# Optimization experiments

Measured on AMD Instinct MI355X. Metric: run time of the kernel, lower is better.

The kernel has to match this reference:

```python
import jax, jax.numpy as jnp
import numpy as np

NUM_C, BS, L, D, M = 4096, 32, 512, 128, 50
TA, TB, TC = 0.075, 0.088, 1.0  # triangular membership params


def setup_inputs() -> dict:
    key = jax.random.key(0)
    ks = jax.random.split(key, 16)
    g = lambda i, shape, s: jax.random.normal(ks[i], shape, jnp.float32) * s
    return {
        "q": jax.random.randint(ks[0], (BS, L), 0, NUM_C),
        "r": jax.random.randint(ks[1], (BS, L), 0, 2),
        "k_emb": g(2, (NUM_C, D), 1.0),
        "Mk": g(3, (M, D), (2.0 / D) ** 0.5),
        "Mv0": g(4, (M, D), (2.0 / D) ** 0.5),
        "f_W": g(5, (D, 2 * D), (1.0 / (2 * D)) ** 0.5),
        "f_b": jnp.zeros((D,), jnp.float32),
        "a_W": g(6, (D, NUM_C + D), (1.0 / (NUM_C + D)) ** 0.5),
        "a_b": jnp.zeros((D,), jnp.float32),
        "e_W": g(7, (D, D), (2.0 / D) ** 0.5),
        "e_b": jnp.zeros((D,), jnp.float32),
        "add_W": g(8, (D, D), (2.0 / D) ** 0.5),
        "add_b": jnp.zeros((D,), jnp.float32),
        "Wih": g(9, (4 * D, D), (1.0 / D) ** 0.5),
        "Whh": g(10, (4 * D, D), (1.0 / D) ** 0.5),
        "bih": jnp.zeros((4 * D,), jnp.float32),
        "bhh": jnp.zeros((4 * D,), jnp.float32),
        "p_W": g(11, (1, D), (1.0 / D) ** 0.5),
        "p_b": jnp.zeros((1,), jnp.float32),
    }


def _forward(q, r, k_emb, Mk, Mv0, f_W, f_b, a_W, a_b, e_W, e_b,
             add_W, add_b, Wih, Whh, bih, bhh, p_W, p_b):
    B, T = q.shape
    k = k_emb[q]                                    # (B,L,D) key embeddings
    # a_embed = Linear(num_c + dim_s, dim_s) on concat(one_hot(q)*r, f):
    # split the weight so the one-hot matmul becomes a gather.
    a_Wq, a_Wf = a_W[:, :NUM_C], a_W[:, NUM_C:]
    yq = a_Wq.T[q] * r[..., None].astype(k.dtype)   # (B,L,D)

    def mem_step(Mv, xs):
        k_t, yq_t = xs                              # (B,D), (B,D)
        w = jax.nn.softmax(k_t @ Mk.T, axis=1)      # (B,M) addressing
        read = jnp.einsum('bm,bmd->bd', w, Mv)      # weighted read
        f = jnp.tanh(jnp.concatenate([read, k_t], 1) @ f_W.T + f_b)
        y = yq_t + f @ a_Wf.T + a_b                 # write content
        e = jax.nn.sigmoid(y @ e_W.T + e_b)         # erase gate
        a = jnp.tanh(y @ add_W.T + add_b)           # add vector
        Mv = Mv * (1.0 - w[:, :, None] * e[:, None, :]) + w[:, :, None] * a[:, None, :]
        return Mv, (w, f)

    Mv0b = jnp.broadcast_to(Mv0, (B, M, D))
    _, (w_all, f_all) = jax.lax.scan(
        mem_step, Mv0b, (k.transpose(1, 0, 2), yq.transpose(1, 0, 2)))
    w_all = w_all.transpose(1, 0, 2)                # (B,L,M)
    f_all = f_all.transpose(1, 0, 2)                # (B,L,D)

    # triangular membership -> ternary identity vectors {0,1,2}
    tw = jnp.maximum(jnp.minimum((w_all - TA) / (TB - TA),
                                 (TC - w_all) / (TC - TB)), 0.0)
    iv = jnp.where(tw >= 0.6, 2.0, jnp.where(tw >= 0.1, 1.0, 0.0))
    sq = jnp.sum(iv * iv, axis=2)                   # (B,L)
    dist = sq[:, :, None] + sq[:, None, :] - 2.0 * jnp.einsum('bim,bjm->bij', iv, iv)
    NEG = jnp.float32(-1e32)
    dist = jnp.where(dist > 0.0, NEG, dist)
    ut = jnp.triu(jnp.ones((T, T), bool), k=0)      # mask j >= i
    dist = jnp.where(ut[None], NEG, dist)
    idx = jnp.arange(T * T, dtype=dist.dtype).reshape(T, T)
    final = dist + idx[None]                        # (B,L,L)
    matched = jnp.max(final, axis=2) >= 0.0         # (B,L) has identical prev step
    prev = jnp.argmax(final, axis=2)                # (B,L) most recent identical t'

    # hop-LSTM: reuse hidden/cell state of previous identical timestep
    barange = jnp.arange(B)
    h0 = jnp.zeros((B, D), k.dtype)
    H0 = jnp.zeros((T, B, D), k.dtype)

    def lstm_step(carry, xs):
        h, c, H, C = carry
        t, f_t, m_t, p_t = xs
        h_in = jnp.where(m_t[:, None], H[p_t, barange], h)
        c_in = jnp.where(m_t[:, None], C[p_t, barange], c)
        gates = f_t @ Wih.T + bih + h_in @ Whh.T + bhh
        i_g, f_g, g_g, o_g = jnp.split(gates, 4, axis=1)  # torch order i,f,g,o
        c_new = jax.nn.sigmoid(f_g) * c_in + jax.nn.sigmoid(i_g) * jnp.tanh(g_g)
        h_new = jax.nn.sigmoid(o_g) * jnp.tanh(c_new)
        return (h_new, c_new, H.at[t].set(h_new), C.at[t].set(c_new)), h_new

    _, h_all = jax.lax.scan(
        lstm_step, (h0, h0, H0, H0),
        (jnp.arange(T), f_all.transpose(1, 0, 2), matched.T, prev.T))
    h_all = h_all.transpose(1, 0, 2)                # (B,L,D)
    # dropout is identity in eval mode
    p = jax.nn.sigmoid(h_all @ p_W.T + p_b)[..., 0]  # (B,L)
    return p


def reference(q, r, k_emb, Mk, Mv0, f_W, f_b, a_W, a_b, e_W, e_b,
              add_W, add_b, Wih, Whh, bih, bhh, p_W, p_b):
    return _forward(q, r, k_emb, Mk, Mv0, f_W, f_b, a_W, a_b, e_W, e_b,
                    add_W, add_b, Wih, Whh, bih, bhh, p_W, p_b)
```

## Files before the change

### kernel.cpp

```cpp
#include <hip/hip_runtime.h>
#include <cstdint>
#include <cstddef>

#define NUM_C 4096
#define BB 32
#define TT 512
#define DD 128
#define MM 50

using ull = unsigned long long;

__device__ __forceinline__ float sigmoidf_(float x){ return 1.0f/(1.0f + expf(-x)); }

__device__ __forceinline__ float fexp2_(float x){ return __builtin_amdgcn_exp2f(x); }
__device__ __forceinline__ float frcp_(float x){ return __builtin_amdgcn_rcpf(x); }
__device__ __forceinline__ float fast_sig_(float x){
  return frcp_(1.0f + fexp2_(-1.44269504088896341f*x));
}
__device__ __forceinline__ float fast_tanh_(float x){
  float t = fexp2_(2.88539008177792681f*x);
  return 1.0f - 2.0f*frcp_(t + 1.0f);
}

__device__ __forceinline__ float quadSum_(float v){
  int t = __builtin_amdgcn_update_dpp(0, __float_as_int(v), 0xB1, 0xF, 0xF, true);
  v += __int_as_float(t);
  t = __builtin_amdgcn_update_dpp(0, __float_as_int(v), 0x4E, 0xF, 0xF, true);
  v += __int_as_float(t);
  return v;
}

__device__ __forceinline__ void barL_(){
  asm volatile("s_waitcnt lgkmcnt(0)\n\ts_barrier" ::: "memory");
}
__device__ __forceinline__ void waitVM_(){
  asm volatile("s_waitcnt vmcnt(0)" ::: "memory");
}

__global__ __launch_bounds__(256) void kPre(
    const int* __restrict__ q, const int* __restrict__ r,
    const float* __restrict__ k_emb, const float* __restrict__ Mk,
    const float* __restrict__ f_W, const float* __restrict__ f_b,
    const float* __restrict__ a_W, const float* __restrict__ a_b,
    float* __restrict__ wAll, ull* __restrict__ keyLo, ull* __restrict__ keyHi,
    float* __restrict__ fpre, float* __restrict__ ypre)
{
  const int b = blockIdx.y, t0 = blockIdx.x * 32, tid = threadIdx.x;
  __shared__ __align__(16) float sK[32*129];
  __shared__ int sQ[32];
  __shared__ int sR[32];
  __shared__ union UU {
    struct { float sMk[MM*129]; double sZ[32*MM]; } p2;
    float sW2[128*65];
  } u;

  if (tid < 32){ sQ[tid] = q[b*TT + t0 + tid]; sR[tid] = r[b*TT + t0 + tid]; }
  __syncthreads();
  for (int i = tid; i < 32*128; i += 256){
    int tl = i >> 7, j = i & 127;
    sK[tl*129 + j] = k_emb[(size_t)sQ[tl]*DD + j];
  }
  for (int i = tid; i < MM*128; i += 256){
    int m = i >> 7, j = i & 127;
    u.p2.sMk[m*129 + j] = Mk[i];
  }
  __syncthreads();

  for (int idx = tid; idx < 32*MM; idx += 256){
    int tl = idx / MM, m = idx - tl*MM;
    double z = 0.0;
    for (int j = 0; j < DD; j++)
      z += (double)sK[tl*129 + j] * (double)u.p2.sMk[m*129 + j];
    u.p2.sZ[tl*MM + m] = z;
  }
  __syncthreads();

  {
    int tl = tid >> 3, l8 = tid & 7;
    double zmax = -1e300;
    for (int m = l8; m < MM; m += 8) zmax = fmax(zmax, u.p2.sZ[tl*MM + m]);
    for (int s = 1; s < 8; s <<= 1) zmax = fmax(zmax, __shfl_xor(zmax, s));
    double se = 0.0;
    for (int m = l8; m < MM; m += 8){
      double e = exp(u.p2.sZ[tl*MM + m] - zmax);
      u.p2.sZ[tl*MM + m] = e;
      se += e;
    }
    for (int s = 1; s < 8; s <<= 1) se += __shfl_xor(se, s);
    double inv = 1.0 / se;
    ull klo = 0, khi = 0;
    for (int m = l8; m < MM; m += 8){
      double w = u.p2.sZ[tl*MM + m] * inv;
      wAll[((size_t)(b*TT + t0 + tl))*MM + m] = (float)w;
      double tw = fmin((w - 0.075)/(0.088 - 0.075), (1.0 - w)/(1.0 - 0.088));
      tw = fmax(tw, 0.0);
      ull iv = (tw >= 0.6) ? 2ull : ((tw >= 0.1) ? 1ull : 0ull);
      if (m < 32) klo |= iv << (2*m); else khi |= iv << (2*(m-32));
    }
    for (int s = 1; s < 8; s <<= 1){ klo |= __shfl_xor(klo, s); khi |= __shfl_xor(khi, s); }
    if (l8 == 0){ keyLo[b*TT + t0 + tl] = klo; keyHi[b*TT + t0 + tl] = khi; }
  }

  {
    const int dq = tid & 31, tq = tid >> 5;
    float acc[4][4];
    #pragma unroll
    for (int a = 0; a < 4; a++){ acc[a][0]=0.f; acc[a][1]=0.f; acc[a][2]=0.f; acc[a][3]=0.f; }
    for (int jh = 0; jh < 2; jh++){
      __syncthreads();
      for (int i = tid; i < 128*64; i += 256){
        int dd = i >> 6, jj = i & 63;
        u.sW2[dd*65 + jj] = f_W[dd*256 + 128 + jh*64 + jj];
      }
      __syncthreads();
      for (int jj = 0; jj < 64; jj++){
        float kv[4], wv[4];
        #pragma unroll
        for (int a = 0; a < 4; a++) kv[a] = sK[(tq*4 + a)*129 + jh*64 + jj];
        #pragma unroll
        for (int c = 0; c < 4; c++) wv[c] = u.sW2[(dq*4 + c)*65 + jj];
        #pragma unroll
        for (int a = 0; a < 4; a++){
          acc[a][0] += kv[a]*wv[0]; acc[a][1] += kv[a]*wv[1];
          acc[a][2] += kv[a]*wv[2]; acc[a][3] += kv[a]*wv[3];
        }
      }
    }
    #pragma unroll
    for (int a = 0; a < 4; a++){
      int tl = tq*4 + a;
      #pragma unroll
      for (int c = 0; c < 4; c++){
        int d = dq*4 + c;
        fpre[((size_t)(b*TT + t0 + tl))*DD + d] = acc[a][c] + f_b[d];
      }
    }
  }

  for (int i = tid; i < 32*DD; i += 256){
    int tl = i >> 7, d = i & 127;
    ypre[((size_t)(b*TT + t0 + tl))*DD + d] =
        a_W[(size_t)d*(NUM_C + DD) + sQ[tl]] * (float)sR[tl] + a_b[d];
  }
}

__global__ __launch_bounds__(256) void kInit(
    const float* __restrict__ e_W, const float* __restrict__ add_W,
    const float* __restrict__ a_W,
    float* __restrict__ Ge, float* __restrict__ Ga,
    const float* __restrict__ Wih, float* __restrict__ Wih4)
{
  const int bx = blockIdx.x, tid = threadIdx.x;
  if (bx < 128){
    __shared__ float se[128];
    __shared__ float sa[128];
    const int d = bx;
    if (tid < 128){
      se[tid] = e_W[(size_t)d*DD + tid];
      sa[tid] = add_W[(size_t)d*DD + tid];
    }
    __syncthreads();
    if (tid < 128){
      const int k = tid;
      float ge = 0.f, ga = 0.f;
      for (int j = 0; j < DD; j++){
        float af = a_W[(size_t)j*(NUM_C + DD) + NUM_C + k];
        ge += se[j]*af;
        ga += sa[j]*af;
      }
      Ge[(size_t)d*DD + k] = ge;
      Ga[(size_t)d*DD + k] = ga;
    }
  } else {
    int idx = (bx - 128)*256 + tid;
    int j = idx >> 7, k = idx & 127;
    Wih4[(size_t)(k >> 2)*2048 + j*4 + (k & 3)] = Wih[idx];
  }
}

__global__ __launch_bounds__(256) void kEA(
    const float* __restrict__ ypre, const float* __restrict__ e_W,
    const float* __restrict__ add_W, const float* __restrict__ e_b,
    const float* __restrict__ add_b, float* __restrict__ eapre)
{
  const int jt = blockIdx.x;
  const int rt = blockIdx.y;
  const int tid = threadIdx.x;
  __shared__ float sW[64*129];
  __shared__ float sF[32*129];
  for (int i = tid; i < 64*128; i += 256){
    int jj = i >> 7, k = i & 127;
    int j = jt*64 + jj;
    sW[jj*129 + k] = (j < 128) ? e_W[(size_t)j*DD + k] : add_W[(size_t)(j-128)*DD + k];
  }
  for (int i = tid; i < 32*128; i += 256){
    int rr = i >> 7, k = i & 127;
    sF[rr*129 + k] = ypre[(size_t)(rt*32 + rr)*DD + k];
  }
  __syncthreads();
  const int jq = tid & 31, rq = tid >> 5;
  float acc[4][2];
  #pragma unroll
  for (int a = 0; a < 4; a++){ acc[a][0] = 0.f; acc[a][1] = 0.f; }
  for (int k = 0; k < 128; k++){
    float fv[4], wv[2];
    #pragma unroll
    for (int a = 0; a < 4; a++) fv[a] = sF[(rq*4 + a)*129 + k];
    wv[0] = sW[(jq*2 + 0)*129 + k];
    wv[1] = sW[(jq*2 + 1)*129 + k];
    #pragma unroll
    for (int a = 0; a < 4; a++){ acc[a][0] += fv[a]*wv[0]; acc[a][1] += fv[a]*wv[1]; }
  }
  #pragma unroll
  for (int a = 0; a < 4; a++){
    int rowi = rt*32 + rq*4 + a;
    #pragma unroll
    for (int c = 0; c < 2; c++){
      int j = jt*64 + jq*2 + c;
      float bj = (j < 128) ? e_b[j] : add_b[j - 128];
      eapre[(size_t)rowi*256 + j] = acc[a][c] + bj;
    }
  }
}

__global__ __launch_bounds__(512, 2) __attribute__((amdgpu_waves_per_eu(2, 2)))
void kFused(
    const float* __restrict__ wAll, const float* __restrict__ fpre,
    const float* __restrict__ eapre, const float* __restrict__ f_W,
    const float* __restrict__ Ge, const float* __restrict__ Ga,
    const float* __restrict__ Mv0, float* __restrict__ fAll,
    const float* __restrict__ Wih4, const float* __restrict__ bih,
    const float* __restrict__ bhh, const ull* __restrict__ keyLo,
    const ull* __restrict__ keyHi, int* __restrict__ prevA,
    const float* __restrict__ Whh, float* __restrict__ Hh,
    float* __restrict__ Ch, float* __restrict__ gpre,
    const float* __restrict__ p_W, const float* __restrict__ p_b,
    float* __restrict__ out, int* __restrict__ prog)
{
  const int tid = threadIdx.x;
  const int b = blockIdx.x & 31;
  const size_t base = (size_t)b*TT;

  __shared__ __align__(16) union SU {
    struct {
      float bufR[144]; float bufF[144]; float sW9[9*52];
      float sF8[8*128]; float sEA8[8*256]; float fO8[8*128];
    } m;
    struct { float sFc[8*128]; ull slo[TT]; ull shi[TT]; } g;
    struct {
      float xh[2][144]; float gbuf[8*512]; int spv[TT];
      float hRing[8*128]; float cRing[8*128]; float pw[DD];
    } l;
  } su;

  if (blockIdx.x < 32){
    const int dd = tid >> 2, kc = tid & 3, m0 = kc*13;
    const int wslot = (dd >> 5)*36 + (dd & 31);

    float mv[13];
    #pragma unroll
    for (int i = 0; i < 13; i++){
      int m = m0 + i;
      mv[i] = (m < MM) ? Mv0[(size_t)m*DD + dd] : 0.f;
    }
    float wf[32], ge[32], ga[32];
    {
      const float4* p;
      p = reinterpret_cast<const float4*>(&f_W[dd*256 + kc*32]);
      #pragma unroll
      for (int i = 0; i < 8; i++){ float4 v = p[i]; wf[4*i]=v.x; wf[4*i+1]=v.y; wf[4*i+2]=v.z; wf[4*i+3]=v.w; }
      p = reinterpret_cast<const float4*>(&Ge[(size_t)dd*DD + kc*32]);
      #pragma unroll
      for (int i = 0; i < 8; i++){ float4 v = p[i]; ge[4*i]=v.x; ge[4*i+1]=v.y; ge[4*i+2]=v.z; ge[4*i+3]=v.w; }
      p = reinterpret_cast<const float4*>(&Ga[(size_t)dd*DD + kc*32]);
      #pragma unroll
      for (int i = 0; i < 8; i++){ float4 v = p[i]; ga[4*i]=v.x; ga[4*i+1]=v.y; ga[4*i+2]=v.z; ga[4*i+3]=v.w; }
    }

    const int rr0 = tid / 50, mm0 = tid - rr0*50;
    if (tid < 18){ int rr = tid >> 1; su.m.sW9[rr*52 + 50 + (tid & 1)] = 0.f; }

    float4 pF = {0.f,0.f,0.f,0.f}, pEA = {0.f,0.f,0.f,0.f};
    float pW = 0.f;
    if (tid < 256) pF = reinterpret_cast<const float4*>(&fpre[base*DD])[tid];
    pEA = reinterpret_cast<const float4*>(&eapre[base*256])[tid];
    if (tid < 450) pW = wAll[(base + rr0)*MM + mm0];

    float wreg[13];

    for (int ch = 0; ch < TT/8; ch++){
      const int t0 = ch*8;
      if (ch){
        if (tid < 256){
          float4 v = reinterpret_cast<const float4*>(su.m.fO8)[tid];
          float* dst = &fAll[(base + t0 - 8)*DD + tid*4];
          __hip_atomic_store(dst+0, v.x, __ATOMIC_RELAXED, __HIP_MEMORY_SCOPE_AGENT);
          __hip_atomic_store(dst+1, v.y, __ATOMIC_RELAXED, __HIP_MEMORY_SCOPE_AGENT);
          __hip_atomic_store(dst+2, v.z, __ATOMIC_RELAXED, __HIP_MEMORY_SCOPE_AGENT);
          __hip_atomic_store(dst+3, v.w, __ATOMIC_RELAXED, __HIP_MEMORY_SCOPE_AGENT);
        }
      }
      if (tid < 256) reinterpret_cast<float4*>(su.m.sF8)[tid] = pF;
      reinterpret_cast<float4*>(su.m.sEA8)[tid] = pEA;
      if (tid < 450) su.m.sW9[rr0*52 + mm0] = pW;
      if (ch && tid < 256) waitVM_();
      if (t0 + 8 < TT){
        if (tid < 256) pF = reinterpret_cast<const float4*>(&fpre[(base + t0 + 8)*DD])[tid];
        pEA = reinterpret_cast<const float4*>(&eapre[(base + t0 + 8)*256])[tid];
        if (tid < 450) pW = (t0 + 8 + rr0 < TT) ? wAll[(base + t0 + 8 + rr0)*MM + mm0] : 0.f;
      }
      barL_();
      if (ch && tid == 0)
        __hip_atomic_store(&prog[b], ch, __ATOMIC_RELAXED, __HIP_MEMORY_SCOPE_AGENT);

      if (ch == 0){
        #pragma unroll
        for (int i = 0; i < 13; i++) wreg[i] = su.m.sW9[m0 + i];
        float r = 0.f;
        #pragma unroll
        for (int i = 0; i < 13; i++) r += wreg[i]*mv[i];
        r = quadSum_(r);
        if (kc == 0) su.m.bufR[wslot] = r;
        barL_();
      }

      #pragma unroll
      for (int tc = 0; tc < 8; tc++){
        float wn[13];
        #pragma unroll
        for (int i = 0; i < 13; i++) wn[i] = su.m.sW9[(tc+1)*52 + m0 + i];

        {
          const float4* x4 = reinterpret_cast<const float4*>(&su.m.bufR[kc*36]);
          float a0=0.f,a1=0.f,a2=0.f,a3=0.f;
          #pragma unroll
          for (int i = 0; i < 8; i++){
            float4 xv = x4[i];
            a0 += xv.x*wf[4*i]; a1 += xv.y*wf[4*i+1]; a2 += xv.z*wf[4*i+2]; a3 += xv.w*wf[4*i+3];
          }
          float s = quadSum_((a0+a1)+(a2+a3));
          float fval = fast_tanh_(s + su.m.sF8[tc*128 + dd]);
          if (kc == 0){
            su.m.bufF[wslot] = fval;
            su.m.fO8[tc*128 + dd] = fval;
          }
        }
        barL_();

        {
          const float4* x4 = reinterpret_cast<const float4*>(&su.m.bufF[kc*36]);
          float e0=0.f,e1=0.f,g0=0.f,g1=0.f;
          #pragma unroll
          for (int i = 0; i < 8; i++){
            float4 xv = x4[i];
            e0 += xv.x*ge[4*i];   e1 += xv.y*ge[4*i+1];
            e0 += xv.z*ge[4*i+2]; e1 += xv.w*ge[4*i+3];
            g0 += xv.x*ga[4*i];   g1 += xv.y*ga[4*i+1];
            g0 += xv.z*ga[4*i+2]; g1 += xv.w*ga[4*i+3];
          }
          float ep = quadSum_(e0 + e1);
          float ap = quadSum_(g0 + g1);
          float e_d = fast_sig_(ep + su.m.sEA8[tc*256 + dd]);
          float a_d = fast_tanh_(ap + su.m.sEA8[tc*256 + 128 + dd]);
          float rp0 = 0.f, rp1 = 0.f;
          #pragma unroll
          for (int i = 0; i < 13; i++){
            float t = __builtin_fmaf(-e_d, mv[i], a_d);
            mv[i] = __builtin_fmaf(wreg[i], t, mv[i]);
            if (i & 1) rp1 = __builtin_fmaf(wn[i], mv[i], rp1);
            else       rp0 = __builtin_fmaf(wn[i], mv[i], rp0);
          }
          float rd = quadSum_(rp0 + rp1);
          if (kc == 0) su.m.bufR[wslot] = rd;
        }
        #pragma unroll
        for (int i = 0; i < 13; i++) wreg[i] = wn[i];
        barL_();
      }
    }

    if (tid < 256){
      float4 v = reinterpret_cast<const float4*>(su.m.fO8)[tid];
      float* dst = &fAll[(base + TT - 8)*DD + tid*4];
      __hip_atomic_store(dst+0, v.x, __ATOMIC_RELAXED, __HIP_MEMORY_SCOPE_AGENT);
      __hip_atomic_store(dst+1, v.y, __ATOMIC_RELAXED, __HIP_MEMORY_SCOPE_AGENT);
      __hip_atomic_store(dst+2, v.z, __ATOMIC_RELAXED, __HIP_MEMORY_SCOPE_AGENT);
      __hip_atomic_store(dst+3, v.w, __ATOMIC_RELAXED, __HIP_MEMORY_SCOPE_AGENT);
      waitVM_();
    }
    __syncthreads();
    if (tid == 0)
      __hip_atomic_store(&prog[b], TT/8, __ATOMIC_RELAXED, __HIP_MEMORY_SCOPE_AGENT);

  } else if (blockIdx.x < 64){
    const float biasj = bih[tid] + bhh[tid];

    {
      su.g.slo[tid] = keyLo[base + tid];
      su.g.shi[tid] = keyHi[base + tid];
      barL_();
      const ull mylo = su.g.slo[tid], myhi = su.g.shi[tid];
      int found = -1;
      for (int j = tid - 1; j >= 0; j--){
        if (su.g.slo[j] == mylo && su.g.shi[j] == myhi){ found = j; break; }
      }
      __hip_atomic_store(&prevA[base + tid], found, __ATOMIC_RELAXED, __HIP_MEMORY_SCOPE_AGENT);
      waitVM_();
    }

    for (int ch = 0; ch < TT/8; ch++){
      const int t0 = ch*8;
      if (tid == 0){
        while (__hip_atomic_load(&prog[b], __ATOMIC_ACQUIRE, __HIP_MEMORY_SCOPE_AGENT) < ch + 1)
          __builtin_amdgcn_s_sleep(2);
      }
      __syncthreads();
      if (tid < 256){
        const float* src = &fAll[(base + t0)*DD + tid*4];
        float x0 = __hip_atomic_load(src+0, __ATOMIC_RELAXED, __HIP_MEMORY_SCOPE_AGENT);
        float x1 = __hip_atomic_load(src+1, __ATOMIC_RELAXED, __HIP_MEMORY_SCOPE_AGENT);
        float x2 = __hip_atomic_load(src+2, __ATOMIC_RELAXED, __HIP_MEMORY_SCOPE_AGENT);
        float x3 = __hip_atomic_load(src+3, __ATOMIC_RELAXED, __HIP_MEMORY_SCOPE_AGENT);
        su.g.sFc[tid*4+0] = x0; su.g.sFc[tid*4+1] = x1;
        su.g.sFc[tid*4+2] = x2; su.g.sFc[tid*4+3] = x3;
      }
      barL_();

      float acc[8];
      #pragma unroll
      for (int u = 0; u < 8; u++) acc[u] = 0.f;
      for (int k4 = 0; k4 < 32; k4++){
        float4 wv = reinterpret_cast<const float4*>(Wih4)[k4*512 + tid];
        #pragma unroll
        for (int u = 0; u < 8; u++){
          float4 fv = *reinterpret_cast<const float4*>(&su.g.sFc[u*128 + k4*4]);
          acc[u] += fv.x*wv.x; acc[u] += fv.y*wv.y;
          acc[u] += fv.z*wv.z; acc[u] += fv.w*wv.w;
        }
      }
      #pragma unroll
      for (int u = 0; u < 8; u++){
        float* dst = &gpre[(base + t0 + u)*512 + tid];
        __hip_atomic_store(dst, acc[u] + biasj, __ATOMIC_RELAXED, __HIP_MEMORY_SCOPE_AGENT);
      }
      waitVM_();
      __syncthreads();
      if (tid == 0)
        __hip_atomic_store(&prog[32 + b], ch + 1, __ATOMIC_RELAXED, __HIP_MEMORY_SCOPE_AGENT);
    }

  } else {
    const int jo = tid >> 2, kc = tid & 3;
    const int wslot = (jo >> 5)*36 + (jo & 31);

    float whh[4][32];
    #pragma unroll
    for (int g = 0; g < 4; g++){
      const float4* W4 = reinterpret_cast<const float4*>(&Whh[(size_t)(g*128 + jo)*128 + kc*32]);
      #pragma unroll
      for (int i = 0; i < 8; i++){
        float4 v = W4[i];
        whh[g][4*i] = v.x; whh[g][4*i+1] = v.y; whh[g][4*i+2] = v.z; whh[g][4*i+3] = v.w;
      }
    }

    float cin_cur = 0.f;

    for (int ch = 0; ch < TT/8; ch++){
      const int t0 = ch*8;
      if (tid == 0){
        while (__hip_atomic_load(&prog[32 + b], __ATOMIC_ACQUIRE, __HIP_MEMORY_SCOPE_AGENT) < ch + 1)
          __builtin_amdgcn_s_sleep(2);
      }
      __syncthreads();
      if (ch == 0){
        su.l.spv[tid] = __hip_atomic_load(&prevA[base + tid], __ATOMIC_RELAXED, __HIP_MEMORY_SCOPE_AGENT);
        if (tid < DD) su.l.xh[0][(tid >> 5)*36 + (tid & 31)] = 0.f;
      }
      {
        const float* src = &gpre[(base + t0)*512 + tid*8];
        float x0 = __hip_atomic_load(src+0, __ATOMIC_RELAXED, __HIP_MEMORY_SCOPE_AGENT);
        float x1 = __hip_atomic_load(src+1, __ATOMIC_RELAXED, __HIP_MEMORY_SCOPE_AGENT);
        float x2 = __hip_atomic_load(src+2, __ATOMIC_RELAXED, __HIP_MEMORY_SCOPE_AGENT);
        float x3 = __hip_atomic_load(src+3, __ATOMIC_RELAXED, __HIP_MEMORY_SCOPE_AGENT);
        float x4 = __hip_atomic_load(src+4, __ATOMIC_RELAXED, __HIP_MEMORY_SCOPE_AGENT);
        float x5 = __hip_atomic_load(src+5, __ATOMIC_RELAXED, __HIP_MEMORY_SCOPE_AGENT);
        float x6 = __hip_atomic_load(src+6, __ATOMIC_RELAXED, __HIP_MEMORY_SCOPE_AGENT);
        float x7 = __hip_atomic_load(src+7, __ATOMIC_RELAXED, __HIP_MEMORY_SCOPE_AGENT);
        float* d = &su.l.gbuf[tid*8];
        d[0]=x0; d[1]=x1; d[2]=x2; d[3]=x3; d[4]=x4; d[5]=x5; d[6]=x6; d[7]=x7;
      }
      barL_();

      #pragma unroll
      for (int tc = 0; tc < 8; tc++){
        const int t = t0 + tc, p = t & 1;
        if (tc) barL_();

        int pv2 = -1; float preH = 0.f, preC = 0.f;
        if (t + 1 < TT){
          pv2 = su.l.spv[t + 1];
          if (pv2 >= 0 && pv2 < t){
            if (pv2 >= t0){
              preH = su.l.hRing[(pv2 & 7)*128 + jo];
              preC = su.l.cRing[(pv2 & 7)*128 + jo];
            } else {
              preH = Hh[(base + pv2)*DD + jo];
              preC = Ch[(base + pv2)*DD + jo];
            }
          }
        }

        float gp0 = su.l.gbuf[tc*512 + jo];
        float gp1 = su.l.gbuf[tc*512 + 128 + jo];
        float gp2 = su.l.gbuf[tc*512 + 256 + jo];
        float gp3 = su.l.gbuf[tc*512 + 384 + jo];

        float a0=0.f,a1=0.f,a2=0.f,a3=0.f;
        {
          const float4* x4 = reinterpret_cast<const float4*>(&su.l.xh[p][kc*36]);
          #pragma unroll
          for (int i = 0; i < 8; i++){
            float4 xv = x4[i];
            a0 += xv.x*whh[0][4*i]; a0 += xv.y*whh[0][4*i+1]; a0 += xv.z*whh[0][4*i+2]; a0 += xv.w*whh[0][4*i+3];
            a1 += xv.x*whh[1][4*i]; a1 += xv.y*whh[1][4*i+1]; a1 += xv.z*whh[1][4*i+2]; a1 += xv.w*whh[1][4*i+3];
            a2 += xv.x*whh[2][4*i]; a2 += xv.y*whh[2][4*i+1]; a2 += xv.z*whh[2][4*i+2]; a2 += xv.w*whh[2][4*i+3];
            a3 += xv.x*whh[3][4*i]; a3 += xv.y*whh[3][4*i+1]; a3 += xv.z*whh[3][4*i+2]; a3 += xv.w*whh[3][4*i+3];
          }
        }
        a0 = quadSum_(a0); a1 = quadSum_(a1); a2 = quadSum_(a2); a3 = quadSum_(a3);

        const float ig = gp0 + a0, fg = gp1 + a1, gg = gp2 + a2, og = gp3 + a3;
        const float cn = fast_sig_(fg)*cin_cur + fast_sig_(ig)*fast_tanh_(gg);
        const float hn = fast_sig_(og)*fast_tanh_(cn);

        if (kc == 0){
          Hh[(base + t)*DD + jo] = hn;
          Ch[(base + t)*DD + jo] = cn;
          su.l.hRing[(t & 7)*128 + jo] = hn;
          su.l.cRing[(t & 7)*128 + jo] = cn;
        }

        float hin_n, cin_n;
        if (pv2 < 0 || pv2 >= t){ hin_n = hn; cin_n = cn; }
        else                     { hin_n = preH; cin_n = preC; }
        if (kc == 0) su.l.xh[1 - p][wslot] = hin_n;
        cin_cur = cin_n;
      }
    }

    __syncthreads();
    if (tid < DD) su.l.pw[tid] = p_W[tid];
    barL_();
    {
      const int t = tid;
      const float* hrow = &Hh[(base + t)*DD];
      float s = 0.f;
      #pragma unroll
      for (int k4 = 0; k4 < 32; k4++){
        float4 hv = *reinterpret_cast<const float4*>(&hrow[k4*4]);
        const float* wp = &su.l.pw[k4*4];
        s += hv.x*wp[0] + hv.y*wp[1] + hv.z*wp[2] + hv.w*wp[3];
      }
      out[base + t] = sigmoidf_(s + p_b[0]);
    }
  }
}

extern "C" void kernel_launch(void* const* d_in, const int* in_sizes, int n_in,
                              void* d_out, int out_size, void* d_ws, size_t ws_size,
                              hipStream_t stream) {
  const int*   q     = (const int*)  d_in[0];
  const int*   r     = (const int*)  d_in[1];
  const float* k_emb = (const float*)d_in[2];
  const float* Mk    = (const float*)d_in[3];
  const float* Mv0   = (const float*)d_in[4];
  const float* f_W   = (const float*)d_in[5];
  const float* f_b   = (const float*)d_in[6];
  const float* a_W   = (const float*)d_in[7];
  const float* a_b   = (const float*)d_in[8];
  const float* e_W   = (const float*)d_in[9];
  const float* e_b   = (const float*)d_in[10];
  const float* add_W = (const float*)d_in[11];
  const float* add_b = (const float*)d_in[12];
  const float* Wih   = (const float*)d_in[13];
  const float* Whh   = (const float*)d_in[14];
  const float* bih   = (const float*)d_in[15];
  const float* bhh   = (const float*)d_in[16];
  const float* p_W   = (const float*)d_in[17];
  const float* p_b   = (const float*)d_in[18];
  float* out = (float*)d_out;

  char* ws = (char*)d_ws;
  size_t off = 0;
  auto alloc = [&](size_t bytes) -> char* {
    char* p = ws + off;
    off += (bytes + 255) & ~(size_t)255;
    return p;
  };
  float* wAll  = (float*)alloc((size_t)BB*TT*MM*4);
  float* fpre  = (float*)alloc((size_t)BB*TT*DD*4);
  float* ypre  = (float*)alloc((size_t)BB*TT*DD*4);
  float* fAll  = (float*)alloc((size_t)BB*TT*DD*4);
  float* eapre = (float*)alloc((size_t)BB*TT*256*4);
  float* gpre  = (float*)alloc((size_t)BB*TT*512*4);
  float* Hh    = (float*)alloc((size_t)BB*TT*DD*4);
  float* Ch    = (float*)alloc((size_t)BB*TT*DD*4);
  ull*   keyLo = (ull*)  alloc((size_t)BB*TT*8);
  ull*   keyHi = (ull*)  alloc((size_t)BB*TT*8);
  int*   prevA = (int*)  alloc((size_t)BB*TT*4);
  float* Ge    = (float*)alloc((size_t)DD*DD*4);
  float* Ga    = (float*)alloc((size_t)DD*DD*4);
  float* Wih4  = (float*)alloc((size_t)512*DD*4);
  int*   prog  = (int*)  alloc(512);
  (void)ws_size; (void)in_sizes; (void)n_in; (void)out_size;

  hipMemsetAsync(prog, 0, 64*sizeof(int), stream);
  kPre  <<<dim3(16, 32), 256, 0, stream>>>(q, r, k_emb, Mk, f_W, f_b, a_W, a_b,
                                           wAll, keyLo, keyHi, fpre, ypre);
  kInit <<<384, 256, 0, stream>>>(e_W, add_W, a_W, Ge, Ga, Wih, Wih4);
  kEA   <<<dim3(4, 512), 256, 0, stream>>>(ypre, e_W, add_W, e_b, add_b, eapre);
  kFused<<<96, 512, 0, stream>>>(wAll, fpre, eapre, f_W, Ge, Ga, Mv0, fAll,
                                 Wih4, bih, bhh, keyLo, keyHi, prevA, Whh,
                                 Hh, Ch, gpre, p_W, p_b, out, prog);
}
```

Before: 758.5 us.

## Fold init and erase/add GEMM into pre/fused kernels with flag-based streaming

Removes the separate kInit and kEA launches and the memset. Weight preprocessing and the prog reset move into an extra row of kPre blocks. The erase/add projection moves into 32 extra producer blocks of kFused, which stream eapre chunk by chunk and publish progress flags that the memory blocks spin on. The LSTM blocks now read gate preactivations directly from global memory, prefetched one step ahead, instead of staging 8 steps in shared memory. This trades launch overhead and serialization for spin-wait synchronization, and it relies on all 128 blocks being co-resident.

```diff
diff --git a/kernel.cpp b/kernel.cpp
--- a/kernel.cpp
+++ b/kernel.cpp
@@ -37,13 +37,24 @@
   asm volatile("s_waitcnt vmcnt(0)" ::: "memory");
 }
 
+__device__ __forceinline__ float agLoad_(const float* p){
+  return __hip_atomic_load(p, __ATOMIC_RELAXED, __HIP_MEMORY_SCOPE_AGENT);
+}
+__device__ __forceinline__ void agStore_(float* p, float v){
+  __hip_atomic_store(p, v, __ATOMIC_RELAXED, __HIP_MEMORY_SCOPE_AGENT);
+}
+
 __global__ __launch_bounds__(256) void kPre(
     const int* __restrict__ q, const int* __restrict__ r,
     const float* __restrict__ k_emb, const float* __restrict__ Mk,
     const float* __restrict__ f_W, const float* __restrict__ f_b,
     const float* __restrict__ a_W, const float* __restrict__ a_b,
     float* __restrict__ wAll, ull* __restrict__ keyLo, ull* __restrict__ keyHi,
-    float* __restrict__ fpre, float* __restrict__ ypre)
+    float* __restrict__ fpre, float* __restrict__ ypre,
+    const float* __restrict__ e_W, const float* __restrict__ add_W,
+    float* __restrict__ Ge, float* __restrict__ Ga,
+    const float* __restrict__ Wih, float* __restrict__ Wih4,
+    int* __restrict__ prog)
 {
   const int b = blockIdx.y, t0 = blockIdx.x * 32, tid = threadIdx.x;
   __shared__ __align__(16) float sK[32*129];
@@ -53,6 +64,42 @@
     struct { float sMk[MM*129]; double sZ[32*MM]; } p2;
     float sW2[128*65];
   } u;
+
+  if (b == 32){
+    const int bx = blockIdx.x;
+    if (bx == 0 && tid < 96) prog[tid] = 0;
+    for (int i = tid; i < 8*128; i += 256){
+      int ld = i >> 7, j = i & 127;
+      sK[i]        = e_W  [(size_t)(bx*8 + ld)*DD + j];
+      sK[1024 + i] = add_W[(size_t)(bx*8 + ld)*DD + j];
+    }
+    __syncthreads();
+    {
+      const int ld = tid >> 5, lane = tid & 31;
+      const int d = bx*8 + ld;
+      float ge[4] = {0.f,0.f,0.f,0.f}, ga[4] = {0.f,0.f,0.f,0.f};
+      for (int j = 0; j < 128; j++){
+        float sej = sK[ld*128 + j], saj = sK[1024 + ld*128 + j];
+        #pragma unroll
+        for (int uu = 0; uu < 4; uu++){
+          float af = a_W[(size_t)j*(NUM_C + DD) + NUM_C + lane + 32*uu];
+          ge[uu] += sej*af;
+          ga[uu] += saj*af;
+        }
+      }
+      #pragma unroll
+      for (int uu = 0; uu < 4; uu++){
+        Ge[(size_t)d*DD + lane + 32*uu] = ge[uu];
+        Ga[(size_t)d*DD + lane + 32*uu] = ga[uu];
+      }
+    }
+    for (int i = tid; i < 4096; i += 256){
+      int idx = bx*4096 + i;
+      int j = idx >> 7, k = idx & 127;
+      Wih4[(size_t)(k >> 2)*2048 + j*4 + (k & 3)] = Wih[idx];
+    }
+    return;
+  }
 
   if (tid < 32){ sQ[tid] = q[b*TT + t0 + tid]; sR[tid] = r[b*TT + t0 + tid]; }
   __syncthreads();
@@ -144,89 +191,10 @@
   }
 }
 
-__global__ __launch_bounds__(256) void kInit(
-    const float* __restrict__ e_W, const float* __restrict__ add_W,
-    const float* __restrict__ a_W,
-    float* __restrict__ Ge, float* __restrict__ Ga,
-    const float* __restrict__ Wih, float* __restrict__ Wih4)
-{
-  const int bx = blockIdx.x, tid = threadIdx.x;
-  if (bx < 128){
-    __shared__ float se[128];
-    __shared__ float sa[128];
-    const int d = bx;
-    if (tid < 128){
-      se[tid] = e_W[(size_t)d*DD + tid];
-      sa[tid] = add_W[(size_t)d*DD + tid];
-    }
-    __syncthreads();
-    if (tid < 128){
-      const int k = tid;
-      float ge = 0.f, ga = 0.f;
-      for (int j = 0; j < DD; j++){
-        float af = a_W[(size_t)j*(NUM_C + DD) + NUM_C + k];
-        ge += se[j]*af;
-        ga += sa[j]*af;
-      }
-      Ge[(size_t)d*DD + k] = ge;
-      Ga[(size_t)d*DD + k] = ga;
-    }
-  } else {
-    int idx = (bx - 128)*256 + tid;
-    int j = idx >> 7, k = idx & 127;
-    Wih4[(size_t)(k >> 2)*2048 + j*4 + (k & 3)] = Wih[idx];
-  }
-}
-
-__global__ __launch_bounds__(256) void kEA(
-    const float* __restrict__ ypre, const float* __restrict__ e_W,
-    const float* __restrict__ add_W, const float* __restrict__ e_b,
-    const float* __restrict__ add_b, float* __restrict__ eapre)
-{
-  const int jt = blockIdx.x;
-  const int rt = blockIdx.y;
-  const int tid = threadIdx.x;
-  __shared__ float sW[64*129];
-  __shared__ float sF[32*129];
-  for (int i = tid; i < 64*128; i += 256){
-    int jj = i >> 7, k = i & 127;
-    int j = jt*64 + jj;
-    sW[jj*129 + k] = (j < 128) ? e_W[(size_t)j*DD + k] : add_W[(size_t)(j-128)*DD + k];
-  }
-  for (int i = tid; i < 32*128; i += 256){
-    int rr = i >> 7, k = i & 127;
-    sF[rr*129 + k] = ypre[(size_t)(rt*32 + rr)*DD + k];
-  }
-  __syncthreads();
-  const int jq = tid & 31, rq = tid >> 5;
-  float acc[4][2];
-  #pragma unroll
-  for (int a = 0; a < 4; a++){ acc[a][0] = 0.f; acc[a][1] = 0.f; }
-  for (int k = 0; k < 128; k++){
-    float fv[4], wv[2];
-    #pragma unroll
-    for (int a = 0; a < 4; a++) fv[a] = sF[(rq*4 + a)*129 + k];
-    wv[0] = sW[(jq*2 + 0)*129 + k];
-    wv[1] = sW[(jq*2 + 1)*129 + k];
-    #pragma unroll
-    for (int a = 0; a < 4; a++){ acc[a][0] += fv[a]*wv[0]; acc[a][1] += fv[a]*wv[1]; }
-  }
-  #pragma unroll
-  for (int a = 0; a < 4; a++){
-    int rowi = rt*32 + rq*4 + a;
-    #pragma unroll
-    for (int c = 0; c < 2; c++){
-      int j = jt*64 + jq*2 + c;
-      float bj = (j < 128) ? e_b[j] : add_b[j - 128];
-      eapre[(size_t)rowi*256 + j] = acc[a][c] + bj;
-    }
-  }
-}
-
 __global__ __launch_bounds__(512, 2) __attribute__((amdgpu_waves_per_eu(2, 2)))
 void kFused(
     const float* __restrict__ wAll, const float* __restrict__ fpre,
-    const float* __restrict__ eapre, const float* __restrict__ f_W,
+    float* __restrict__ eapre, const float* __restrict__ f_W,
     const float* __restrict__ Ge, const float* __restrict__ Ga,
     const float* __restrict__ Mv0, float* __restrict__ fAll,
     const float* __restrict__ Wih4, const float* __restrict__ bih,
@@ -235,7 +203,10 @@
     const float* __restrict__ Whh, float* __restrict__ Hh,
     float* __restrict__ Ch, float* __restrict__ gpre,
     const float* __restrict__ p_W, const float* __restrict__ p_b,
-    float* __restrict__ out, int* __restrict__ prog)
+    float* __restrict__ out, int* __restrict__ prog,
+    const float* __restrict__ ypre, const float* __restrict__ e_W,
+    const float* __restrict__ add_W, const float* __restrict__ e_b,
+    const float* __restrict__ add_b)
 {
   const int tid = threadIdx.x;
   const int b = blockIdx.x & 31;
@@ -248,12 +219,47 @@
     } m;
     struct { float sFc[8*128]; ull slo[TT]; ull shi[TT]; } g;
     struct {
-      float xh[2][144]; float gbuf[8*512]; int spv[TT];
+      float xh[2][144]; int spv[TT];
       float hRing[8*128]; float cRing[8*128]; float pw[DD];
     } l;
+    struct { float sY[8*128]; } e;
   } su;
 
-  if (blockIdx.x < 32){
+  if (blockIdx.x >= 96){
+    const int j  = tid & 255;
+    const int rg = tid >> 8;
+    const float* wcol = (j < 128) ? &e_W[(size_t)j*DD] : &add_W[(size_t)(j-128)*DD];
+    const float bias  = (j < 128) ? e_b[j] : add_b[j - 128];
+    const float4* wcol4 = reinterpret_cast<const float4*>(wcol);
+
+    for (int ch = 0; ch < TT/8; ch++){
+      const int t0 = ch*8;
+      if (ch) __syncthreads();
+      if (tid < 256){
+        float4 v = reinterpret_cast<const float4*>(&ypre[(base + t0)*DD])[tid];
+        reinterpret_cast<float4*>(su.e.sY)[tid] = v;
+      }
+      barL_();
+      float acc[4] = {0.f,0.f,0.f,0.f};
+      for (int k4 = 0; k4 < 32; k4++){
+        float4 w = wcol4[k4];
+        #pragma unroll
+        for (int uu = 0; uu < 4; uu++){
+          const float* y = &su.e.sY[(rg + 2*uu)*128 + k4*4];
+          acc[uu] += y[0]*w.x; acc[uu] += y[1]*w.y;
+          acc[uu] += y[2]*w.z; acc[uu] += y[3]*w.w;
+        }
+      }
+      #pragma unroll
+      for (int uu = 0; uu < 4; uu++)
+        agStore_(&eapre[(base + t0 + rg + 2*uu)*256 + j], acc[uu] + bias);
+      waitVM_();
+      __syncthreads();
+      if (tid == 0)
+        __hip_atomic_store(&prog[64 + b], ch + 1, __ATOMIC_RELAXED, __HIP_MEMORY_SCOPE_AGENT);
+    }
+
+  } else if (blockIdx.x < 32){
     const int dd = tid >> 2, kc = tid & 3, m0 = kc*13;
     const int wslot = (dd >> 5)*36 + (dd & 31);
 
@@ -280,11 +286,18 @@
     const int rr0 = tid / 50, mm0 = tid - rr0*50;
     if (tid < 18){ int rr = tid >> 1; su.m.sW9[rr*52 + 50 + (tid & 1)] = 0.f; }
 
-    float4 pF = {0.f,0.f,0.f,0.f}, pEA = {0.f,0.f,0.f,0.f};
+    float4 pF = {0.f,0.f,0.f,0.f};
+    float pEA0 = 0.f, pEA1 = 0.f, pEA2 = 0.f, pEA3 = 0.f;
     float pW = 0.f;
     if (tid < 256) pF = reinterpret_cast<const float4*>(&fpre[base*DD])[tid];
-    pEA = reinterpret_cast<const float4*>(&eapre[base*256])[tid];
     if (tid < 450) pW = wAll[(base + rr0)*MM + mm0];
+    while (__hip_atomic_load(&prog[64 + b], __ATOMIC_ACQUIRE, __HIP_MEMORY_SCOPE_AGENT) < 1)
+      __builtin_amdgcn_s_sleep(2);
+    {
+      const float* ep = &eapre[base*256 + tid*4];
+      pEA0 = agLoad_(ep+0); pEA1 = agLoad_(ep+1);
+      pEA2 = agLoad_(ep+2); pEA3 = agLoad_(ep+3);
+    }
 
     float wreg[13];
 
@@ -294,33 +307,39 @@
         if (tid < 256){
           float4 v = reinterpret_cast<const float4*>(su.m.fO8)[tid];
           float* dst = &fAll[(base + t0 - 8)*DD + tid*4];
-          __hip_atomic_store(dst+0, v.x, __ATOMIC_RELAXED, __HIP_MEMORY_SCOPE_AGENT);
-          __hip_atomic_store(dst+1, v.y, __ATOMIC_RELAXED, __HIP_MEMORY_SCOPE_AGENT);
-          __hip_atomic_store(dst+2, v.z, __ATOMIC_RELAXED, __HIP_MEMORY_SCOPE_AGENT);
-          __hip_atomic_store(dst+3, v.w, __ATOMIC_RELAXED, __HIP_MEMORY_SCOPE_AGENT);
+          agStore_(dst+0, v.x); agStore_(dst+1, v.y);
+          agStore_(dst+2, v.z); agStore_(dst+3, v.w);
         }
       }
       if (tid < 256) reinterpret_cast<float4*>(su.m.sF8)[tid] = pF;
-      reinterpret_cast<float4*>(su.m.sEA8)[tid] = pEA;
+      su.m.sEA8[tid*4+0] = pEA0; su.m.sEA8[tid*4+1] = pEA1;
+      su.m.sEA8[tid*4+2] = pEA2; su.m.sEA8[tid*4+3] = pEA3;
       if (tid < 450) su.m.sW9[rr0*52 + mm0] = pW;
       if (ch && tid < 256) waitVM_();
       if (t0 + 8 < TT){
         if (tid < 256) pF = reinterpret_cast<const float4*>(&fpre[(base + t0 + 8)*DD])[tid];
-        pEA = reinterpret_cast<const float4*>(&eapre[(base + t0 + 8)*256])[tid];
         if (tid < 450) pW = (t0 + 8 + rr0 < TT) ? wAll[(base + t0 + 8 + rr0)*MM + mm0] : 0.f;
       }
       barL_();
       if (ch && tid == 0)
         __hip_atomic_store(&prog[b], ch, __ATOMIC_RELAXED, __HIP_MEMORY_SCOPE_AGENT);
 
+      if (t0 + 8 < TT){
+        while (__hip_atomic_load(&prog[64 + b], __ATOMIC_ACQUIRE, __HIP_MEMORY_SCOPE_AGENT) < ch + 2)
+          __builtin_amdgcn_s_sleep(2);
+        const float* ep = &eapre[(base + t0 + 8)*256 + tid*4];
+        pEA0 = agLoad_(ep+0); pEA1 = agLoad_(ep+1);
+        pEA2 = agLoad_(ep+2); pEA3 = agLoad_(ep+3);
+      }
+
       if (ch == 0){
         #pragma unroll
         for (int i = 0; i < 13; i++) wreg[i] = su.m.sW9[m0 + i];
-        float r = 0.f;
-        #pragma unroll
-        for (int i = 0; i < 13; i++) r += wreg[i]*mv[i];
-        r = quadSum_(r);
-        if (kc == 0) su.m.bufR[wslot] = r;
+        float rr = 0.f;
+        #pragma unroll
+        for (int i = 0; i < 13; i++) rr += wreg[i]*mv[i];
+        rr = quadSum_(rr);
+        if (kc == 0) su.m.bufR[wslot] = rr;
         barL_();
       }
 
@@ -382,10 +401,8 @@
     if (tid < 256){
       float4 v = reinterpret_cast<const float4*>(su.m.fO8)[tid];
       float* dst = &fAll[(base + TT - 8)*DD + tid*4];
-      __hip_atomic_store(dst+0, v.x, __ATOMIC_RELAXED, __HIP_MEMORY_SCOPE_AGENT);
-      __hip_atomic_store(dst+1, v.y, __ATOMIC_RELAXED, __HIP_MEMORY_SCOPE_AGENT);
-      __hip_atomic_store(dst+2, v.z, __ATOMIC_RELAXED, __HIP_MEMORY_SCOPE_AGENT);
-      __hip_atomic_store(dst+3, v.w, __ATOMIC_RELAXED, __HIP_MEMORY_SCOPE_AGENT);
+      agStore_(dst+0, v.x); agStore_(dst+1, v.y);
+      agStore_(dst+2, v.z); agStore_(dst+3, v.w);
       waitVM_();
     }
     __syncthreads();
@@ -417,10 +434,8 @@
       __syncthreads();
       if (tid < 256){
         const float* src = &fAll[(base + t0)*DD + tid*4];
-        float x0 = __hip_atomic_load(src+0, __ATOMIC_RELAXED, __HIP_MEMORY_SCOPE_AGENT);
-        float x1 = __hip_atomic_load(src+1, __ATOMIC_RELAXED, __HIP_MEMORY_SCOPE_AGENT);
-        float x2 = __hip_atomic_load(src+2, __ATOMIC_RELAXED, __HIP_MEMORY_SCOPE_AGENT);
-        float x3 = __hip_atomic_load(src+3, __ATOMIC_RELAXED, __HIP_MEMORY_SCOPE_AGENT);
+        float x0 = agLoad_(src+0), x1 = agLoad_(src+1);
+        float x2 = agLoad_(src+2), x3 = agLoad_(src+3);
         su.g.sFc[tid*4+0] = x0; su.g.sFc[tid*4+1] = x1;
         su.g.sFc[tid*4+2] = x2; su.g.sFc[tid*4+3] = x3;
       }
@@ -428,21 +443,19 @@
 
       float acc[8];
       #pragma unroll
-      for (int u = 0; u < 8; u++) acc[u] = 0.f;
+      for (int uu = 0; uu < 8; uu++) acc[uu] = 0.f;
       for (int k4 = 0; k4 < 32; k4++){
         float4 wv = reinterpret_cast<const float4*>(Wih4)[k4*512 + tid];
         #pragma unroll
-        for (int u = 0; u < 8; u++){
-          float4 fv = *reinterpret_cast<const float4*>(&su.g.sFc[u*128 + k4*4]);
-          acc[u] += fv.x*wv.x; acc[u] += fv.y*wv.y;
-          acc[u] += fv.z*wv.z; acc[u] += fv.w*wv.w;
-        }
-      }
-      #pragma unroll
-      for (int u = 0; u < 8; u++){
-        float* dst = &gpre[(base + t0 + u)*512 + tid];
-        __hip_atomic_store(dst, acc[u] + biasj, __ATOMIC_RELAXED, __HIP_MEMORY_SCOPE_AGENT);
-      }
+        for (int uu = 0; uu < 8; uu++){
+          float4 fv = *reinterpret_cast<const float4*>(&su.g.sFc[uu*128 + k4*4]);
+          acc[uu] += fv.x*wv.x; acc[uu] += fv.y*wv.y;
+          acc[uu] += fv.z*wv.z; acc[uu] += fv.w*wv.w;
+        }
+      }
+      #pragma unroll
+      for (int uu = 0; uu < 8; uu++)
+        agStore_(&gpre[(base + t0 + uu)*512 + tid], acc[uu] + biasj);
       waitVM_();
       __syncthreads();
       if (tid == 0)
@@ -477,20 +490,13 @@
         su.l.spv[tid] = __hip_atomic_load(&prevA[base + tid], __ATOMIC_RELAXED, __HIP_MEMORY_SCOPE_AGENT);
         if (tid < DD) su.l.xh[0][(tid >> 5)*36 + (tid & 31)] = 0.f;
       }
+      float g0, g1, g2, g3;
       {
-        const float* src = &gpre[(base + t0)*512 + tid*8];
-        float x0 = __hip_atomic_load(src+0, __ATOMIC_RELAXED, __HIP_MEMORY_SCOPE_AGENT);
-        float x1 = __hip_atomic_load(src+1, __ATOMIC_RELAXED, __HIP_MEMORY_SCOPE_AGENT);
-        float x2 = __hip_atomic_load(src+2, __ATOMIC_RELAXED, __HIP_MEMORY_SCOPE_AGENT);
-        float x3 = __hip_atomic_load(src+3, __ATOMIC_RELAXED, __HIP_MEMORY_SCOPE_AGENT);
-        float x4 = __hip_atomic_load(src+4, __ATOMIC_RELAXED, __HIP_MEMORY_SCOPE_AGENT);
-        float x5 = __hip_atomic_load(src+5, __ATOMIC_RELAXED, __HIP_MEMORY_SCOPE_AGENT);
-        float x6 = __hip_atomic_load(src+6, __ATOMIC_RELAXED, __HIP_MEMORY_SCOPE_AGENT);
-        float x7 = __hip_atomic_load(src+7, __ATOMIC_RELAXED, __HIP_MEMORY_SCOPE_AGENT);
-        float* d = &su.l.gbuf[tid*8];
-        d[0]=x0; d[1]=x1; d[2]=x2; d[3]=x3; d[4]=x4; d[5]=x5; d[6]=x6; d[7]=x7;
-      }
-      barL_();
+        const float* gp = &gpre[(base + t0)*512 + jo];
+        g0 = agLoad_(gp);       g1 = agLoad_(gp + 128);
+        g2 = agLoad_(gp + 256); g3 = agLoad_(gp + 384);
+      }
+      if (ch == 0) barL_();
 
       #pragma unroll
       for (int tc = 0; tc < 8; tc++){
@@ -510,11 +516,12 @@
             }
           }
         }
-
-        float gp0 = su.l.gbuf[tc*512 + jo];
-        float gp1 = su.l.gbuf[tc*512 + 128 + jo];
-        float gp2 = su.l.gbuf[tc*512 + 256 + jo];
-        float gp3 = su.l.gbuf[tc*512 + 384 + jo];
+        float n0 = 0.f, n1 = 0.f, n2 = 0.f, n3 = 0.f;
+        if (tc < 7){
+          const float* gp = &gpre[(base + t + 1)*512 + jo];
+          n0 = agLoad_(gp);       n1 = agLoad_(gp + 128);
+          n2 = agLoad_(gp + 256); n3 = agLoad_(gp + 384);
+        }
 
         float a0=0.f,a1=0.f,a2=0.f,a3=0.f;
         {
@@ -530,7 +537,7 @@
         }
         a0 = quadSum_(a0); a1 = quadSum_(a1); a2 = quadSum_(a2); a3 = quadSum_(a3);
 
-        const float ig = gp0 + a0, fg = gp1 + a1, gg = gp2 + a2, og = gp3 + a3;
+        const float ig = g0 + a0, fg = g1 + a1, gg = g2 + a2, og = g3 + a3;
         const float cn = fast_sig_(fg)*cin_cur + fast_sig_(ig)*fast_tanh_(gg);
         const float hn = fast_sig_(og)*fast_tanh_(cn);
 
@@ -546,6 +553,7 @@
         else                     { hin_n = preH; cin_n = preC; }
         if (kc == 0) su.l.xh[1 - p][wslot] = hin_n;
         cin_cur = cin_n;
+        g0 = n0; g1 = n1; g2 = n2; g3 = n3;
       }
     }
 
@@ -615,12 +623,11 @@
   int*   prog  = (int*)  alloc(512);
   (void)ws_size; (void)in_sizes; (void)n_in; (void)out_size;
 
-  hipMemsetAsync(prog, 0, 64*sizeof(int), stream);
-  kPre  <<<dim3(16, 32), 256, 0, stream>>>(q, r, k_emb, Mk, f_W, f_b, a_W, a_b,
-                                           wAll, keyLo, keyHi, fpre, ypre);
-  kInit <<<384, 256, 0, stream>>>(e_W, add_W, a_W, Ge, Ga, Wih, Wih4);
-  kEA   <<<dim3(4, 512), 256, 0, stream>>>(ypre, e_W, add_W, e_b, add_b, eapre);
-  kFused<<<96, 512, 0, stream>>>(wAll, fpre, eapre, f_W, Ge, Ga, Mv0, fAll,
-                                 Wih4, bih, bhh, keyLo, keyHi, prevA, Whh,
-                                 Hh, Ch, gpre, p_W, p_b, out, prog);
-}
+  kPre  <<<dim3(16, 33), 256, 0, stream>>>(q, r, k_emb, Mk, f_W, f_b, a_W, a_b,
+                                           wAll, keyLo, keyHi, fpre, ypre,
+                                           e_W, add_W, Ge, Ga, Wih, Wih4, prog);
+  kFused<<<128, 512, 0, stream>>>(wAll, fpre, eapre, f_W, Ge, Ga, Mv0, fAll,
+                                  Wih4, bih, bhh, keyLo, keyHi, prevA, Whh,
+                                  Hh, Ch, gpre, p_W, p_b, out, prog,
+                                  ypre, e_W, add_W, e_b, add_b);
+}
```

After: 830.2 us. 9.5% more time.
